# Performance work log

Measured on AMD Instinct MI355X. Metric: run time of the kernel, lower is better.

## Reference

```python
import jax, jax.numpy as jnp
import numpy as np

H = 1024          # hidden_size
NH = 16           # num_attention_heads
HD = H // NH      # head_dim = 64
FF = 4096         # intermediate_size
EPS = 1e-12       # layer_norm_eps
CLAMP = 1e9


def _layer_norm(x, gamma, beta):
    mu = jnp.mean(x, axis=-1, keepdims=True)
    var = jnp.mean(jnp.square(x - mu), axis=-1, keepdims=True)
    return (x - mu) * jax.lax.rsqrt(var + EPS) * gamma + beta


def setup_inputs() -> dict:
    key = jax.random.key(0)
    ks = jax.random.split(key, 12)
    B, S = 4, 2048
    s_h = 1.0 / np.sqrt(H)
    s_f = 1.0 / np.sqrt(FF)
    return {
        "hidden_states": jax.random.normal(ks[0], (B, S, H), jnp.float32),
        "Wq": jax.random.normal(ks[1], (H, H), jnp.float32) * s_h,
        "bq": jnp.zeros((H,), jnp.float32),
        "Wk": jax.random.normal(ks[2], (H, H), jnp.float32) * s_h,
        "bk": jnp.zeros((H,), jnp.float32),
        "Wv": jax.random.normal(ks[3], (H, H), jnp.float32) * s_h,
        "bv": jnp.zeros((H,), jnp.float32),
        "ln1_g": jnp.ones((H,), jnp.float32),
        "ln1_b": jnp.zeros((H,), jnp.float32),
        "W1": jax.random.normal(ks[4], (H, FF), jnp.float32) * s_h,
        "b1": jnp.zeros((FF,), jnp.float32),
        "W2": jax.random.normal(ks[5], (FF, H), jnp.float32) * s_f,
        "b2": jnp.zeros((H,), jnp.float32),
        "ln2_g": jnp.ones((H,), jnp.float32),
        "ln2_b": jnp.zeros((H,), jnp.float32),
    }


def reference(hidden_states, Wq, bq, Wk, bk, Wv, bv, ln1_g, ln1_b,
              W1, b1, W2, b2, ln2_g, ln2_b):
    B, S, _ = hidden_states.shape
    # QKV projections -> [B, NH, S, HD]
    def heads(x):
        return x.reshape(B, S, NH, HD).transpose(0, 2, 1, 3)
    q = heads(hidden_states @ Wq + bq)
    k = heads(hidden_states @ Wk + bk)
    v = heads(hidden_states @ Wv + bv)
    # manual attention: scale, clamp, softmax + 1e-9 epsilon
    scores = jnp.einsum('bhqd,bhkd->bhqk', q, k) / np.sqrt(HD)
    scores = jnp.clip(scores, -CLAMP, CLAMP)
    probs = jax.nn.softmax(scores, axis=-1) + 1e-9
    ctx = jnp.einsum('bhqk,bhkd->bhqd', probs, v)
    ctx = ctx.transpose(0, 2, 1, 3).reshape(B, S, NH * HD)
    # residual + LN (no output projection in this module)
    x = _layer_norm(hidden_states + ctx, ln1_g, ln1_b)
    # FFN with exact gelu + clamp
    inter = jax.nn.gelu(x @ W1 + b1, approximate=False)
    inter = jnp.clip(inter, -CLAMP, CLAMP)
    out = inter @ W2 + b2
    return _layer_norm(out + x, ln2_g, ln2_b)
```

## Files before the change

kernel.cpp:

```cpp
#include <hip/hip_runtime.h>
#include <math.h>


#define H_   1024
#define NH_  16
#define HD_  64
#define FF_  4096
#define S_   2048
#define B_   4
#define BS_  (B_ * S_)

#define EPI_NONE 0
#define EPI_GELU 1
#define EPI_QKV3 2

typedef unsigned short ushort_t;
typedef short v8s __attribute__((ext_vector_type(8)));
typedef float v4f __attribute__((ext_vector_type(4)));
typedef float v16f __attribute__((ext_vector_type(16)));

#define CQ_ 0.18033688011112042f

__device__ __forceinline__ unsigned short f2bf(float f) {
    union { float f; unsigned int u; } v; v.f = f;
    unsigned int u = v.u;
    return (unsigned short)((u + 0x7fffu + ((u >> 16) & 1u)) >> 16);
}
__device__ __forceinline__ float bf2f(unsigned short h) {
    union { unsigned int u; float f; } v; v.u = ((unsigned int)h) << 16;
    return v.f;
}

__device__ __forceinline__ unsigned cvt_pk_bf16(float lo, float hi) {
    unsigned r;
    asm("v_cvt_pk_bf16_f32 %0, %1, %2" : "=v"(r) : "v"(lo), "v"(hi));
    return r;
}
__device__ __forceinline__ void pl32_swap(unsigned &a, unsigned &b) {
    asm("v_permlane32_swap_b32 %0, %1" : "+v"(a), "+v"(b));
}

typedef __attribute__((address_space(1))) void gvoid;
typedef __attribute__((address_space(3))) void lvoid;
__device__ __forceinline__ void async16(const void* g, void* l) {
    __builtin_amdgcn_global_load_lds((gvoid*)g, (lvoid*)l, 16, 0, 0);
}

__device__ __forceinline__ float gelu_fast(float x) {
    const float x2 = x * x;
    const float w  = fmaf(x2, 0.044715f, 1.0f);
    const float e  = __builtin_exp2f(x * w * -2.3022083f);
    return x * __builtin_amdgcn_rcpf(1.0f + e);
}

__global__ __launch_bounds__(256)
void cast_bf16_kernel(const float* __restrict__ x, ushort_t* __restrict__ y)
{
    const size_t i = ((size_t)blockIdx.x * 256 + threadIdx.x) * 4;
    float4 v = *(const float4*)&x[i];
    ushort4 o;
    o.x = f2bf(v.x); o.y = f2bf(v.y); o.z = f2bf(v.z); o.w = f2bf(v.w);
    *(ushort4*)&y[i] = o;
}

__global__ __launch_bounds__(256)
void cast_transpose_kernel(const float* __restrict__ W, ushort_t* __restrict__ Wt,
                           int K, int N)
{
    __shared__ float tile[32][33];
    const int tid = threadIdx.x;
    const int n0 = blockIdx.x * 32, k0 = blockIdx.y * 32;
    const int r  = tid >> 3;
    const int c4 = (tid & 7) * 4;
    float4 v = *(const float4*)&W[(size_t)(k0 + r) * N + n0 + c4];
    tile[r][c4 + 0] = v.x; tile[r][c4 + 1] = v.y;
    tile[r][c4 + 2] = v.z; tile[r][c4 + 3] = v.w;
    __syncthreads();
    ushort4 o;
    o.x = f2bf(tile[c4 + 0][r]); o.y = f2bf(tile[c4 + 1][r]);
    o.z = f2bf(tile[c4 + 2][r]); o.w = f2bf(tile[c4 + 3][r]);
    *(ushort4*)&Wt[(size_t)(n0 + r) * K + k0 + c4] = o;
}

__global__ __launch_bounds__(256)
void concat3_kernel(const float* __restrict__ a, const float* __restrict__ b,
                    const float* __restrict__ c, float* __restrict__ o)
{
    const int i = blockIdx.x * 256 + threadIdx.x;
    o[i] = (i < 1024) ? a[i] : (i < 2048) ? b[i - 1024] : c[i - 2048];
}

template <int EPI>
__global__ __launch_bounds__(256)
void bgemm_kernel(const ushort_t* __restrict__ A, const ushort_t* __restrict__ Bt,
                  const float* __restrict__ bias, void* __restrict__ Cout,
                  int M, int N, int K)
{
    __shared__ ushort_t Atile[2 * 128 * 32];
    __shared__ ushort_t Btile[2 * 128 * 32];

    const int tid  = threadIdx.x;
    const int wave = tid >> 6;
    const int lane = tid & 63;
    const int m    = lane & 31;
    const int hi   = lane >> 5;
    const int wm   = wave >> 1, wn = wave & 1;
    const int blockM = blockIdx.y * 128;
    const int blockN = blockIdx.x * 128;

    v16f acc[2][2];
#pragma unroll
    for (int a = 0; a < 2; ++a)
#pragma unroll
        for (int b = 0; b < 2; ++b) acc[a][b] = (v16f)0.f;

    auto stage = [&](int buf, int ktile) {
        const int kt = ktile * 32;
#pragma unroll
        for (int i = 0; i < 2; ++i) {
            const int chunk = i * 256 + tid;
            const int row = chunk >> 2;
            const int g   = (chunk & 3) ^ (((row >> 1) ^ (row >> 3)) & 3);
            async16(A  + (size_t)(blockM + row) * K + kt + g * 8,
                    &Atile[buf * 4096 + chunk * 8]);
            async16(Bt + (size_t)(blockN + row) * K + kt + g * 8,
                    &Btile[buf * 4096 + chunk * 8]);
        }
    };

    const int sw = ((m >> 1) ^ (m >> 3)) & 3;
    auto compute = [&](int buf) {
        v8s af[2][2], bfr[2][2];
#pragma unroll
        for (int w = 0; w < 2; ++w) {
            const int slot = ((w * 2 + hi) ^ sw) * 8;
#pragma unroll
            for (int f = 0; f < 2; ++f) {
                af[w][f]  = *(const v8s*)&Atile[buf * 4096 + (wm * 64 + f * 32 + m) * 32 + slot];
                bfr[w][f] = *(const v8s*)&Btile[buf * 4096 + (wn * 64 + f * 32 + m) * 32 + slot];
            }
        }
        __builtin_amdgcn_s_setprio(1);
#pragma unroll
        for (int w = 0; w < 2; ++w)
#pragma unroll
            for (int a = 0; a < 2; ++a)
#pragma unroll
                for (int b = 0; b < 2; ++b)
                    acc[a][b] = __builtin_amdgcn_mfma_f32_32x32x16_bf16(
                        af[w][a], bfr[w][b], acc[a][b], 0, 0, 0);
        __builtin_amdgcn_s_setprio(0);
    };

    const int NT = K >> 5;

    stage(0, 0);
    asm volatile("s_waitcnt vmcnt(0)" ::: "memory");
    __builtin_amdgcn_s_barrier();
    __builtin_amdgcn_sched_barrier(0);

    for (int t = 0; t < NT; ++t) {
        if (t + 1 < NT) stage((t + 1) & 1, t + 1);
        compute(t & 1);
        if (t < NT - 1) {
            asm volatile("s_waitcnt lgkmcnt(0)" ::: "memory");
            asm volatile("s_waitcnt vmcnt(0)" ::: "memory");
            __builtin_amdgcn_s_barrier();
            __builtin_amdgcn_sched_barrier(0);
        }
    }

#pragma unroll
    for (int im = 0; im < 2; ++im) {
#pragma unroll
        for (int in = 0; in < 2; ++in) {
            const int n  = blockN + wn * 64 + in * 32 + m;
            const float bn = bias[n];
            if (EPI == EPI_QKV3) {
                const int nn = n & 1023;
                const int hh = nn >> 6, dd = nn & 63;
                ushort_t* base = (ushort_t*)Cout + (size_t)(n >> 10) * ((size_t)BS_ * H_);
                if (n < 2048) {
                    const float sc = (n < 1024) ? CQ_ : 1.f;
#pragma unroll
                    for (int g = 0; g < 4; ++g)
#pragma unroll
                        for (int rr = 0; rr < 4; ++rr) {
                            const int mr = blockM + wm * 64 + im * 32 + g * 8 + hi * 4 + rr;
                            base[(((size_t)((mr >> 11) * NH_ + hh)) * S_ + (mr & 2047)) * HD_ + dd]
                                = f2bf((acc[im][in][g * 4 + rr] + bn) * sc);
                        }
                } else {
#pragma unroll
                    for (int g = 0; g < 4; ++g) {
                        const int m0 = blockM + wm * 64 + im * 32 + g * 8 + hi * 4;
                        ushort4 pk;
                        pk.x = f2bf(acc[im][in][g * 4 + 0] + bn);
                        pk.y = f2bf(acc[im][in][g * 4 + 1] + bn);
                        pk.z = f2bf(acc[im][in][g * 4 + 2] + bn);
                        pk.w = f2bf(acc[im][in][g * 4 + 3] + bn);
                        *(ushort4*)&base[(((size_t)((m0 >> 11) * NH_ + hh)) * HD_ + dd) * S_
                                         + (m0 & 2047)] = pk;
                    }
                }
            } else {
#pragma unroll
                for (int g = 0; g < 4; ++g)
#pragma unroll
                    for (int rr = 0; rr < 4; ++rr) {
                        const int mr = blockM + wm * 64 + im * 32 + g * 8 + hi * 4 + rr;
                        float v = acc[im][in][g * 4 + rr] + bn;
                        if (EPI == EPI_GELU) {
                            ((ushort_t*)Cout)[(size_t)mr * N + n] = f2bf(gelu_fast(v));
                        } else {
                            ((float*)Cout)[(size_t)mr * N + n] = v;
                        }
                    }
            }
        }
    }
}

__global__ __launch_bounds__(256)
void vsum_kernel(const ushort_t* __restrict__ VT, float* __restrict__ vsum)
{
    const int bh   = blockIdx.x;
    const int tid  = threadIdx.x;
    const int d    = tid >> 2;
    const int part = tid & 3;
    const ushort_t* p = VT + (size_t)bh * HD_ * S_ + (size_t)d * S_ + part * 512;
    float acc = 0.f;
    for (int i = 0; i < 512; i += 4) {
        ushort4 u = *(const ushort4*)&p[i];
        acc += (bf2f(u.x) + bf2f(u.y)) + (bf2f(u.z) + bf2f(u.w));
    }
    acc += __shfl_xor(acc, 1);
    acc += __shfl_xor(acc, 2);
    if (part == 0) vsum[bh * HD_ + d] = acc;
}

__global__ __launch_bounds__(256)
void flash_kernel(const ushort_t* __restrict__ Q, const ushort_t* __restrict__ Kg,
                  const ushort_t* __restrict__ VT, const float* __restrict__ vsum,
                  float* __restrict__ ctx)
{
    __shared__ ushort_t smem[16384];

    int wg = blockIdx.x;
    wg = (wg & 7) * 128 + (wg >> 3);
    const int bh = wg >> 4;
    const int q0 = (wg & 15) * 128;

    const int tid  = threadIdx.x;
    const int wave = tid >> 6;
    const int lane = tid & 63;
    const int m    = lane & 31;
    const int hi   = lane >> 5;

    const ushort_t* Qp = Q  + (size_t)bh * S_ * HD_ + (size_t)q0 * HD_;
    const ushort_t* Kp = Kg + (size_t)bh * S_ * HD_;
    const ushort_t* Vp = VT + (size_t)bh * HD_ * S_;

    ushort_t* Qs = &smem[8192];

    auto stageKV = [&](int buf, int t) {
        const int kv0 = t * 64;
        ushort_t* Ksb = &smem[buf * 8192];
        ushort_t* Vsb = &smem[buf * 8192 + 4096];
#pragma unroll
        for (int i = 0; i < 2; ++i) {
            const int ch = i * 256 + tid;
            const int row = ch >> 3, c = ch & 7;
            async16(Kp + (size_t)(kv0 + row) * HD_ + ((c ^ (row & 7)) * 8),
                    &Ksb[ch * 8]);
            async16(Vp + (size_t)row * S_ + kv0 + ((c ^ (row & 7)) * 8),
                    &Vsb[ch * 8]);
        }
    };

#pragma unroll
    for (int i = 0; i < 4; ++i) {
        const int ch = i * 256 + tid;
        const int row = ch >> 3, c = ch & 7;
        async16(Qp + (size_t)row * HD_ + ((c ^ (row & 7)) * 8), &Qs[ch * 8]);
    }
    stageKV(0, 0);
    asm volatile("s_waitcnt vmcnt(0)" ::: "memory");
    __builtin_amdgcn_s_barrier();
    __builtin_amdgcn_sched_barrier(0);

    v8s qf[4];
    {
        const int qrow = wave * 32 + m;
#pragma unroll
        for (int c = 0; c < 4; ++c)
            qf[c] = *(const v8s*)&Qs[qrow * 64 + (((2 * c + hi) ^ (qrow & 7)) * 8)];
    }
    asm volatile("s_waitcnt lgkmcnt(0)" ::: "memory");
    __builtin_amdgcn_s_barrier();
    __builtin_amdgcn_sched_barrier(0);

    v16f o0 = (v16f)0.f, o1 = (v16f)0.f;
    float lp0 = 0.f, lp1 = 0.f, lp2 = 0.f, lp3 = 0.f;
    v8s pf[4];

    const int NT = S_ / 64;
    for (int t = 0; t < NT; ++t) {
        const int b = t & 1;
        if (t + 1 < NT) stageKV(b ^ 1, t + 1);
        const ushort_t* Ksb = &smem[b * 8192];
        const ushort_t* Vsb = &smem[b * 8192 + 4096];

#pragma unroll
        for (int a = 0; a < 2; ++a) {
            v16f z = (v16f)0.f;
            const int krow = a * 32 + m;
#pragma unroll
            for (int c = 0; c < 4; ++c) {
                v8s kf = *(const v8s*)&Ksb[krow * 64 + (((2 * c + hi) ^ (m & 7)) * 8)];
                z = __builtin_amdgcn_mfma_f32_32x32x16_bf16(kf, qf[c], z, 0, 0, 0);
            }
            unsigned u[8];
#pragma unroll
            for (int mm = 0; mm < 8; ++mm) {
                const float plo = __builtin_exp2f(z[2 * mm]);
                const float phi = __builtin_exp2f(z[2 * mm + 1]);
                if ((mm & 3) == 0)      lp0 += plo + phi;
                else if ((mm & 3) == 1) lp1 += plo + phi;
                else if ((mm & 3) == 2) lp2 += plo + phi;
                else                    lp3 += plo + phi;
                u[mm] = cvt_pk_bf16(plo, phi);
            }
            pl32_swap(u[0], u[2]); pl32_swap(u[1], u[3]);
            pl32_swap(u[4], u[6]); pl32_swap(u[5], u[7]);
            union { unsigned w[4]; v8s s; } c0, c1;
            c0.w[0] = u[0]; c0.w[1] = u[1]; c0.w[2] = u[2]; c0.w[3] = u[3];
            c1.w[0] = u[4]; c1.w[1] = u[5]; c1.w[2] = u[6]; c1.w[3] = u[7];
            pf[2 * a]     = c0.s;
            pf[2 * a + 1] = c1.s;
        }

#pragma unroll
        for (int c = 0; c < 4; ++c) {
            const int sw = ((2 * c + hi) ^ (m & 7)) * 8;
            v8s vf0 = *(const v8s*)&Vsb[m * 64 + sw];
            v8s vf1 = *(const v8s*)&Vsb[(32 + m) * 64 + sw];
            o0 = __builtin_amdgcn_mfma_f32_32x32x16_bf16(vf0, pf[c], o0, 0, 0, 0);
            o1 = __builtin_amdgcn_mfma_f32_32x32x16_bf16(vf1, pf[c], o1, 0, 0, 0);
        }

        asm volatile("s_waitcnt lgkmcnt(0)" ::: "memory");
        asm volatile("s_waitcnt vmcnt(0)" ::: "memory");
        __builtin_amdgcn_s_barrier();
        __builtin_amdgcn_sched_barrier(0);
    }

    float l_r = (lp0 + lp1) + (lp2 + lp3);
    l_r += __shfl_xor(l_r, 32);
    const float linv = 1.f / l_r;

    const int bb = bh >> 4, hh = bh & 15;
    const int srow = q0 + wave * 32 + m;
    float* cp = ctx + ((size_t)(bb * S_ + srow)) * H_ + hh * HD_;
#pragma unroll
    for (int g = 0; g < 2; ++g) {
        const v16f& o = g ? o1 : o0;
#pragma unroll
        for (int rq = 0; rq < 4; ++rq) {
            const int d0 = g * 32 + rq * 8 + hi * 4;
            float4 vs4 = *(const float4*)&vsum[bh * HD_ + d0];
            float4 ov;
            ov.x = o[rq * 4 + 0] * linv + 1e-9f * vs4.x;
            ov.y = o[rq * 4 + 1] * linv + 1e-9f * vs4.y;
            ov.z = o[rq * 4 + 2] * linv + 1e-9f * vs4.z;
            ov.w = o[rq * 4 + 3] * linv + 1e-9f * vs4.w;
            *(float4*)&cp[d0] = ov;
        }
    }
}

template <bool WB>
__global__ __launch_bounds__(256)
void add_ln_kernel(const float* __restrict__ A, const float* __restrict__ Bv,
                   const float* __restrict__ gamma, const float* __restrict__ beta,
                   float* __restrict__ out, ushort_t* __restrict__ outb)
{
    const int row = blockIdx.x;
    const int tid = threadIdx.x;
    const float* a = A  + (size_t)row * H_;
    const float* b = Bv + (size_t)row * H_;

    float4 av = *(const float4*)&a[tid * 4];
    float4 bv = *(const float4*)&b[tid * 4];
    float x[4] = { av.x + bv.x, av.y + bv.y, av.z + bv.z, av.w + bv.w };

    float s  = x[0] + x[1] + x[2] + x[3];
    float s2 = x[0]*x[0] + x[1]*x[1] + x[2]*x[2] + x[3]*x[3];
#pragma unroll
    for (int off = 1; off < 64; off <<= 1) {
        s  += __shfl_xor(s,  off);
        s2 += __shfl_xor(s2, off);
    }
    __shared__ float rs[8];
    const int wave = tid >> 6, lane = tid & 63;
    if (lane == 0) { rs[wave] = s; rs[4 + wave] = s2; }
    __syncthreads();
    const float sum  = rs[0] + rs[1] + rs[2] + rs[3];
    const float sum2 = rs[4] + rs[5] + rs[6] + rs[7];
    const float mu   = sum * (1.f / H_);
    const float var  = sum2 * (1.f / H_) - mu * mu;
    const float rstd = rsqrtf(var + 1e-12f);

    float4 gv = *(const float4*)&gamma[tid * 4];
    float4 be = *(const float4*)&beta[tid * 4];
    float4 ov;
    ov.x = (x[0] - mu) * rstd * gv.x + be.x;
    ov.y = (x[1] - mu) * rstd * gv.y + be.y;
    ov.z = (x[2] - mu) * rstd * gv.z + be.z;
    ov.w = (x[3] - mu) * rstd * gv.w + be.w;
    *(float4*)&out[(size_t)row * H_ + tid * 4] = ov;
    if (WB) {
        ushort4 ob;
        ob.x = f2bf(ov.x); ob.y = f2bf(ov.y); ob.z = f2bf(ov.z); ob.w = f2bf(ov.w);
        *(ushort4*)&outb[(size_t)row * H_ + tid * 4] = ob;
    }
}

extern "C" void kernel_launch(void* const* d_in, const int* in_sizes, int n_in,
                              void* d_out, int out_size, void* d_ws, size_t ws_size,
                              hipStream_t stream)
{
    const float* hidden = (const float*)d_in[0];
    const float* Wq     = (const float*)d_in[1];
    const float* bq     = (const float*)d_in[2];
    const float* Wk     = (const float*)d_in[3];
    const float* bk     = (const float*)d_in[4];
    const float* Wv     = (const float*)d_in[5];
    const float* bv     = (const float*)d_in[6];
    const float* ln1_g  = (const float*)d_in[7];
    const float* ln1_b  = (const float*)d_in[8];
    const float* W1     = (const float*)d_in[9];
    const float* b1     = (const float*)d_in[10];
    const float* W2     = (const float*)d_in[11];
    const float* b2     = (const float*)d_in[12];
    const float* ln2_g  = (const float*)d_in[13];
    const float* ln2_b  = (const float*)d_in[14];

    char* ws = (char*)d_ws;
    const size_t MB = 1024 * 1024;
    ushort_t* Xb    = (ushort_t*)(ws + 0);
    ushort_t* x1b   = (ushort_t*)(ws + 0);
    ushort_t* Wqt   = (ushort_t*)(ws + 16 * MB);
    ushort_t* Wkt   = (ushort_t*)(ws + 18 * MB);
    ushort_t* Wvt   = (ushort_t*)(ws + 20 * MB);
    ushort_t* W1t   = (ushort_t*)(ws + 16 * MB);
    ushort_t* W2t   = (ushort_t*)(ws + 24 * MB);
    ushort_t* q     = (ushort_t*)(ws + 32 * MB);
    ushort_t* k     = (ushort_t*)(ws + 48 * MB);
    ushort_t* vt    = (ushort_t*)(ws + 64 * MB);
    float*    ctx   = (float*)(ws + 80 * MB);
    ushort_t* inter = (ushort_t*)(ws + 32 * MB);
    float*    bcat  = (float*)(ws + 96 * MB);
    float*    vsum  = (float*)(ws + 96 * MB + 16384);
    float*    out2  = (float*)(ws + 96 * MB);
    float*    x1    = (float*)(ws + 128 * MB);
    float*    out   = (float*)d_out;

    const dim3 blk(256);

    cast_bf16_kernel<<<dim3(BS_ * H_ / 1024), blk, 0, stream>>>(hidden, Xb);
    cast_transpose_kernel<<<dim3(32, 32),  blk, 0, stream>>>(Wq, Wqt, H_, H_);
    cast_transpose_kernel<<<dim3(32, 32),  blk, 0, stream>>>(Wk, Wkt, H_, H_);
    cast_transpose_kernel<<<dim3(32, 32),  blk, 0, stream>>>(Wv, Wvt, H_, H_);
    cast_transpose_kernel<<<dim3(32, 128), blk, 0, stream>>>(W2, W2t, FF_, H_);
    concat3_kernel<<<dim3(12), blk, 0, stream>>>(bq, bk, bv, bcat);

    bgemm_kernel<EPI_QKV3><<<dim3(24, 64), blk, 0, stream>>>(
        Xb, Wqt, bcat, q, BS_, 3 * H_, H_);

    cast_transpose_kernel<<<dim3(128, 32), blk, 0, stream>>>(W1, W1t, H_, FF_);

    vsum_kernel<<<dim3(B_ * NH_), blk, 0, stream>>>(vt, vsum);

    flash_kernel<<<dim3((S_ / 128) * (B_ * NH_)), blk, 0, stream>>>(q, k, vt, vsum, ctx);

    add_ln_kernel<true><<<dim3(BS_), blk, 0, stream>>>(hidden, ctx, ln1_g, ln1_b, x1, x1b);

    bgemm_kernel<EPI_GELU><<<dim3(32, 64), blk, 0, stream>>>(x1b, W1t, b1, inter, BS_, FF_, H_);

    bgemm_kernel<EPI_NONE><<<dim3(8, 64), blk, 0, stream>>>(inter, W2t, b2, out2, BS_, H_, FF_);

    add_ln_kernel<false><<<dim3(BS_), blk, 0, stream>>>(out2, x1, ln2_g, ln2_b, out, nullptr);
}
```

Measured before the change: 592.5 us.

## Triple-buffer GEMM prefetch and split-K the FFN down-projection with atomics

The bf16 GEMM kernel moves from double to triple buffering in LDS, issuing loads two k-tiles ahead and waiting on only the older tile's loads (vmcnt(4)), so global latency is better hidden. The W2 GEMM (K=4096, only 512 blocks) is split into two K halves across blockIdx.z and accumulates into a pre-zeroed fp32 buffer with atomicAdd, which doubles the block count for better CU occupancy. The b2 bias moves into the final add+LayerNorm kernel. In exchange it adds a zeroing pass, atomic traffic, summation order that is no longer deterministic, and 50% more LDS per block, which may lower occupancy.

```diff
diff --git a/kernel.cpp b/kernel.cpp
--- a/kernel.cpp
+++ b/kernel.cpp
@@ -10,7 +10,7 @@
 #define B_   4
 #define BS_  (B_ * S_)
 
-#define EPI_NONE 0
+#define EPI_ATOM 0
 #define EPI_GELU 1
 #define EPI_QKV3 2
 
@@ -61,6 +61,12 @@
     ushort4 o;
     o.x = f2bf(v.x); o.y = f2bf(v.y); o.z = f2bf(v.z); o.w = f2bf(v.w);
     *(ushort4*)&y[i] = o;
+}
+
+__global__ __launch_bounds__(256)
+void zero_kernel(float4* __restrict__ p)
+{
+    p[(size_t)blockIdx.x * 256 + threadIdx.x] = make_float4(0.f, 0.f, 0.f, 0.f);
 }
 
 __global__ __launch_bounds__(256)
@@ -94,10 +100,10 @@
 __global__ __launch_bounds__(256)
 void bgemm_kernel(const ushort_t* __restrict__ A, const ushort_t* __restrict__ Bt,
                   const float* __restrict__ bias, void* __restrict__ Cout,
-                  int M, int N, int K)
-{
-    __shared__ ushort_t Atile[2 * 128 * 32];
-    __shared__ ushort_t Btile[2 * 128 * 32];
+                  int M, int N, int Keff, int lda, int ldb)
+{
+    __shared__ ushort_t Atile[3 * 128 * 32];
+    __shared__ ushort_t Btile[3 * 128 * 32];
 
     const int tid  = threadIdx.x;
     const int wave = tid >> 6;
@@ -107,6 +113,7 @@
     const int wm   = wave >> 1, wn = wave & 1;
     const int blockM = blockIdx.y * 128;
     const int blockN = blockIdx.x * 128;
+    const int koff   = blockIdx.z * Keff;
 
     v16f acc[2][2];
 #pragma unroll
@@ -115,15 +122,15 @@
         for (int b = 0; b < 2; ++b) acc[a][b] = (v16f)0.f;
 
     auto stage = [&](int buf, int ktile) {
-        const int kt = ktile * 32;
+        const int kt = koff + ktile * 32;
 #pragma unroll
         for (int i = 0; i < 2; ++i) {
             const int chunk = i * 256 + tid;
             const int row = chunk >> 2;
             const int g   = (chunk & 3) ^ (((row >> 1) ^ (row >> 3)) & 3);
-            async16(A  + (size_t)(blockM + row) * K + kt + g * 8,
+            async16(A  + (size_t)(blockM + row) * lda + kt + g * 8,
                     &Atile[buf * 4096 + chunk * 8]);
-            async16(Bt + (size_t)(blockN + row) * K + kt + g * 8,
+            async16(Bt + (size_t)(blockN + row) * ldb + kt + g * 8,
                     &Btile[buf * 4096 + chunk * 8]);
         }
     };
@@ -152,19 +159,27 @@
         __builtin_amdgcn_s_setprio(0);
     };
 
-    const int NT = K >> 5;
+    const int NT = Keff >> 5;
 
     stage(0, 0);
-    asm volatile("s_waitcnt vmcnt(0)" ::: "memory");
+    stage(1, 1);
+    asm volatile("s_waitcnt vmcnt(4)" ::: "memory");
     __builtin_amdgcn_s_barrier();
     __builtin_amdgcn_sched_barrier(0);
 
+    int bc = 0, bs = 2;
     for (int t = 0; t < NT; ++t) {
-        if (t + 1 < NT) stage((t + 1) & 1, t + 1);
-        compute(t & 1);
+        const bool more = (t + 2 < NT);
+        if (more) {
+            stage(bs, t + 2);
+            bs = (bs == 2) ? 0 : bs + 1;
+        }
+        compute(bc);
+        bc = (bc == 2) ? 0 : bc + 1;
         if (t < NT - 1) {
             asm volatile("s_waitcnt lgkmcnt(0)" ::: "memory");
-            asm volatile("s_waitcnt vmcnt(0)" ::: "memory");
+            if (more) asm volatile("s_waitcnt vmcnt(4)" ::: "memory");
+            else      asm volatile("s_waitcnt vmcnt(0)" ::: "memory");
             __builtin_amdgcn_s_barrier();
             __builtin_amdgcn_sched_barrier(0);
         }
@@ -175,7 +190,7 @@
 #pragma unroll
         for (int in = 0; in < 2; ++in) {
             const int n  = blockN + wn * 64 + in * 32 + m;
-            const float bn = bias[n];
+            const float bn = (EPI == EPI_ATOM) ? 0.f : bias[n];
             if (EPI == EPI_QKV3) {
                 const int nn = n & 1023;
                 const int hh = nn >> 6, dd = nn & 63;
@@ -209,11 +224,11 @@
 #pragma unroll
                     for (int rr = 0; rr < 4; ++rr) {
                         const int mr = blockM + wm * 64 + im * 32 + g * 8 + hi * 4 + rr;
-                        float v = acc[im][in][g * 4 + rr] + bn;
+                        const float v = acc[im][in][g * 4 + rr] + bn;
                         if (EPI == EPI_GELU) {
                             ((ushort_t*)Cout)[(size_t)mr * N + n] = f2bf(gelu_fast(v));
                         } else {
-                            ((float*)Cout)[(size_t)mr * N + n] = v;
+                            atomicAdd(&((float*)Cout)[(size_t)mr * N + n], v);
                         }
                     }
             }
@@ -379,9 +394,10 @@
     }
 }
 
-template <bool WB>
+template <bool WB, bool HASB>
 __global__ __launch_bounds__(256)
 void add_ln_kernel(const float* __restrict__ A, const float* __restrict__ Bv,
+                   const float* __restrict__ bias2,
                    const float* __restrict__ gamma, const float* __restrict__ beta,
                    float* __restrict__ out, ushort_t* __restrict__ outb)
 {
@@ -393,6 +409,10 @@
     float4 av = *(const float4*)&a[tid * 4];
     float4 bv = *(const float4*)&b[tid * 4];
     float x[4] = { av.x + bv.x, av.y + bv.y, av.z + bv.z, av.w + bv.w };
+    if (HASB) {
+        float4 b4 = *(const float4*)&bias2[tid * 4];
+        x[0] += b4.x; x[1] += b4.y; x[2] += b4.z; x[3] += b4.w;
+    }
 
     float s  = x[0] + x[1] + x[2] + x[3];
     float s2 = x[0]*x[0] + x[1]*x[1] + x[2]*x[2] + x[3]*x[3];
@@ -476,7 +496,7 @@
     concat3_kernel<<<dim3(12), blk, 0, stream>>>(bq, bk, bv, bcat);
 
     bgemm_kernel<EPI_QKV3><<<dim3(24, 64), blk, 0, stream>>>(
-        Xb, Wqt, bcat, q, BS_, 3 * H_, H_);
+        Xb, Wqt, bcat, q, BS_, 3 * H_, H_, H_, H_);
 
     cast_transpose_kernel<<<dim3(128, 32), blk, 0, stream>>>(W1, W1t, H_, FF_);
 
@@ -484,11 +504,17 @@
 
     flash_kernel<<<dim3((S_ / 128) * (B_ * NH_)), blk, 0, stream>>>(q, k, vt, vsum, ctx);
 
-    add_ln_kernel<true><<<dim3(BS_), blk, 0, stream>>>(hidden, ctx, ln1_g, ln1_b, x1, x1b);
-
-    bgemm_kernel<EPI_GELU><<<dim3(32, 64), blk, 0, stream>>>(x1b, W1t, b1, inter, BS_, FF_, H_);
-
-    bgemm_kernel<EPI_NONE><<<dim3(8, 64), blk, 0, stream>>>(inter, W2t, b2, out2, BS_, H_, FF_);
-
-    add_ln_kernel<false><<<dim3(BS_), blk, 0, stream>>>(out2, x1, ln2_g, ln2_b, out, nullptr);
-}
+    add_ln_kernel<true, false><<<dim3(BS_), blk, 0, stream>>>(
+        hidden, ctx, nullptr, ln1_g, ln1_b, x1, x1b);
+
+    zero_kernel<<<dim3(BS_ * H_ * 4 / (256 * 16)), blk, 0, stream>>>((float4*)out2);
+
+    bgemm_kernel<EPI_GELU><<<dim3(32, 64), blk, 0, stream>>>(
+        x1b, W1t, b1, inter, BS_, FF_, H_, H_, H_);
+
+    bgemm_kernel<EPI_ATOM><<<dim3(8, 64, 2), blk, 0, stream>>>(
+        inter, W2t, b2, out2, BS_, H_, FF_ / 2, FF_, FF_);
+
+    add_ln_kernel<false, true><<<dim3(BS_), blk, 0, stream>>>(
+        out2, x1, b2, ln2_g, ln2_b, out, nullptr);
+}
```

Measured after the change: 631.6 us. 6.6% more time.
